# Kernel optimization log

Measured on AMD Instinct MI355X. Metric: run time of the kernel, lower is better.

Reference implementation:

```python
import jax, jax.numpy as jnp
import numpy as np

B, S, D = 32, 1024, 1024


def setup_inputs() -> dict:
    key = jax.random.key(0)
    ks = jax.random.split(key, 4)
    scale = 1.0 / np.sqrt(D)
    x = jax.random.normal(ks[0], (B, S, D), dtype=jnp.float32)
    Wg = jax.random.normal(ks[1], (D, D), dtype=jnp.float32) * scale
    Ws = jax.random.normal(ks[2], (D, D), dtype=jnp.float32) * scale
    Wi = jax.random.normal(ks[3], (D, D), dtype=jnp.float32) * scale
    bg = jnp.zeros((D,), jnp.float32)
    bs = jnp.zeros((D,), jnp.float32)
    bi = jnp.zeros((D,), jnp.float32)
    return {"x": x, "Wg": Wg, "bg": bg, "Ws": Ws, "bs": bs, "Wi": Wi, "bi": bi}


def reference(x, Wg, bg, Ws, bs, Wi, bi):
    # ContractiveSequenceMixer scan:
    #   gate_t = sigmoid(x_t @ Wg.T + bg)        (input-only: precomputable)
    #   mix_t  = h @ Ws.T + bs + (x_t @ Wi.T + bi)
    #   h      = gate_t * mix_t + (1 - gate_t) * h
    #   emit_t = h
    gates = jax.nn.sigmoid(jnp.einsum('bsd,ed->bse', x, Wg) + bg)  # [B,S,D]
    pin = jnp.einsum('bsd,ed->bse', x, Wi) + bi                     # [B,S,D]

    def step(state, gp):
        g, p = gp  # each [B, D]
        mix = state @ Ws.T + bs + p
        next_state = g * mix + (1.0 - g) * state
        return next_state, next_state

    init = jnp.zeros((x.shape[0], x.shape[2]), x.dtype)
    # time-major for scan
    final_state, outs = jax.lax.scan(
        step, init, (jnp.swapaxes(gates, 0, 1), jnp.swapaxes(pin, 0, 1)))
    emitted = jnp.swapaxes(outs, 0, 1)  # [B, S, D]
    return emitted, final_state
```

## Files before the change

kernel.cpp:

```cpp
#include <hip/hip_runtime.h>
#include <cstdint>


#define BATCH 32
#define SEQ   1024
#define DIM   1024
static const size_t BSD = (size_t)BATCH * SEQ * DIM;

typedef short  s16x8 __attribute__((ext_vector_type(8)));
typedef unsigned short u16x4 __attribute__((ext_vector_type(4)));
typedef float  f32x4 __attribute__((ext_vector_type(4)));

__device__ __forceinline__ unsigned short f2bf(float f) {
  union { float f; unsigned int u; } v; v.f = f;
  unsigned int r = v.u + 0x7fffu + ((v.u >> 16) & 1u);
  return (unsigned short)(r >> 16);
}
__device__ __forceinline__ float bf2f(unsigned short h) {
  union { unsigned int u; float f; } v; v.u = ((unsigned int)h) << 16; return v.f;
}

__device__ __forceinline__ void gload_lds16(const void* g, void* l) {
  __builtin_amdgcn_global_load_lds(
      (const __attribute__((address_space(1))) void*)g,
      (__attribute__((address_space(3))) void*)l, 16, 0, 0);
}

#define HLOAD(dst, base, IMM)                                              \
  asm volatile("global_load_dwordx4 %0, %1, off offset:" IMM " sc0 sc1"    \
               : "=v"(dst) : "v"(base))
#define HL8(arr, base)        \
  HLOAD(arr[0], base, "0");   \
  HLOAD(arr[1], base, "64");  \
  HLOAD(arr[2], base, "128"); \
  HLOAD(arr[3], base, "192"); \
  HLOAD(arr[4], base, "256"); \
  HLOAD(arr[5], base, "320"); \
  HLOAD(arr[6], base, "384"); \
  HLOAD(arr[7], base, "448")

__device__ __forceinline__ void cstore8(void* p, u16x4 v) {
  asm volatile("global_store_dwordx2 %0, %1, off sc0 sc1"
               :: "v"(p), "v"(v) : "memory");
}
__device__ __forceinline__ void cstore4(void* p, int v) {
  asm volatile("global_store_dword %0, %1, off sc0 sc1"
               :: "v"(p), "v"(v) : "memory");
}
__device__ __forceinline__ void cstore4u(void* p, unsigned v) {
  asm volatile("global_store_dword %0, %1, off sc0 sc1"
               :: "v"(p), "v"(v) : "memory");
}
__device__ __forceinline__ int cload4(const void* p) {
  int v;
  asm volatile("global_load_dword %0, %1, off sc0 sc1\n\ts_waitcnt vmcnt(0)"
               : "=v"(v) : "v"(p) : "memory");
  return v;
}

__global__ void split_x_kernel(const float* __restrict__ x,
                               unsigned short* __restrict__ xh,
                               unsigned short* __restrict__ xl, long n4) {
  long i = (long)blockIdx.x * blockDim.x + threadIdx.x;
  const long stride = (long)gridDim.x * blockDim.x;
  for (; i < n4; i += stride) {
    f32x4 v = *(const f32x4*)&x[i * 4];
    u16x4 vh, vl;
#pragma unroll
    for (int j = 0; j < 4; ++j) {
      unsigned short hb = f2bf(v[j]);
      vh[j] = hb; vl[j] = f2bf(v[j] - bf2f(hb));
    }
    *(u16x4*)&xh[i * 4] = vh;
    *(u16x4*)&xl[i * 4] = vl;
  }
}

__global__ void split_w_kernel(const float* __restrict__ Wg,
                               const float* __restrict__ Wi,
                               unsigned short* __restrict__ wh,
                               unsigned short* __restrict__ wl) {
  long i = (long)blockIdx.x * blockDim.x + threadIdx.x;
  if (i >= (long)(2048 * 1024 / 4)) return;
  long flat = i * 4;
  int row = (int)(flat >> 10);
  int col = (int)(flat & 1023);
  const float* src = (row < 1024) ? &Wg[(size_t)row * 1024 + col]
                                  : &Wi[(size_t)(row - 1024) * 1024 + col];
  f32x4 v = *(const f32x4*)src;
  u16x4 vh, vl;
#pragma unroll
  for (int j = 0; j < 4; ++j) {
    unsigned short hb = f2bf(v[j]);
    vh[j] = hb; vl[j] = f2bf(v[j] - bf2f(hb));
  }
  *(u16x4*)&wh[flat] = vh;
  *(u16x4*)&wl[flat] = vl;
}

__global__ void init_kernel(unsigned short* h_hi, unsigned short* h_lo,
                            int* flags) {
  int i = blockIdx.x * blockDim.x + threadIdx.x;
  u16x4 z4 = {0, 0, 0, 0};
  if (i < 16384) {
    cstore8(h_hi + (size_t)i * 4, z4);
    cstore8(h_lo + (size_t)i * 4, z4);
  }
  if (i < 4096) cstore4(flags + i, 0);
}

__global__ __launch_bounds__(256) void gemm_gp_kernel(
    const unsigned short* __restrict__ xh, const unsigned short* __restrict__ xl,
    const unsigned short* __restrict__ wh, const unsigned short* __restrict__ wl,
    const float* __restrict__ bg, const float* __restrict__ bi,
    float* __restrict__ G, float* __restrict__ P) {
  __shared__ unsigned short sAh[128 * 32], sAl[128 * 32], sBh[128 * 32], sBl[128 * 32];
  const int tid = threadIdx.x;
  const int w = tid >> 6, l = tid & 63;
  const int wr = w >> 1, wc = w & 1;
  const int lr = l & 15, lk8 = (l >> 4) * 8;
  const size_t rBase = (size_t)blockIdx.x * 128;
  const int cBase = blockIdx.y * 128;

  f32x4 acc[4][4];
  f32x4 z = {0.f, 0.f, 0.f, 0.f};
#pragma unroll
  for (int m = 0; m < 4; ++m)
#pragma unroll
    for (int n = 0; n < 4; ++n) acc[m][n] = z;

  for (int kb = 0; kb < 32; ++kb) {
    const int k0 = kb * 32;
#pragma unroll
    for (int i = 0; i < 2; ++i) {
      const int chunk = w * 128 + i * 64 + l;
      const int row = chunk >> 2;
      const int c8 = (chunk & 3) * 8;
      gload_lds16(xh + (rBase + row) * 1024 + k0 + c8, &sAh[chunk * 8]);
      gload_lds16(xl + (rBase + row) * 1024 + k0 + c8, &sAl[chunk * 8]);
      gload_lds16(wh + (size_t)(cBase + row) * 1024 + k0 + c8, &sBh[chunk * 8]);
      gload_lds16(wl + (size_t)(cBase + row) * 1024 + k0 + c8, &sBl[chunk * 8]);
    }
    __syncthreads();

    s16x8 ah[4], al[4], bh[4], bl[4];
#pragma unroll
    for (int m = 0; m < 4; ++m) {
      ah[m] = *(const s16x8*)&sAh[(wr * 64 + m * 16 + lr) * 32 + lk8];
      al[m] = *(const s16x8*)&sAl[(wr * 64 + m * 16 + lr) * 32 + lk8];
    }
#pragma unroll
    for (int n = 0; n < 4; ++n) {
      bh[n] = *(const s16x8*)&sBh[(wc * 64 + n * 16 + lr) * 32 + lk8];
      bl[n] = *(const s16x8*)&sBl[(wc * 64 + n * 16 + lr) * 32 + lk8];
    }
#pragma unroll
    for (int m = 0; m < 4; ++m)
#pragma unroll
      for (int n = 0; n < 4; ++n)
        acc[m][n] = __builtin_amdgcn_mfma_f32_16x16x32_bf16(ah[m], bh[n], acc[m][n], 0, 0, 0);
#pragma unroll
    for (int m = 0; m < 4; ++m)
#pragma unroll
      for (int n = 0; n < 4; ++n)
        acc[m][n] = __builtin_amdgcn_mfma_f32_16x16x32_bf16(al[m], bh[n], acc[m][n], 0, 0, 0);
#pragma unroll
    for (int m = 0; m < 4; ++m)
#pragma unroll
      for (int n = 0; n < 4; ++n)
        acc[m][n] = __builtin_amdgcn_mfma_f32_16x16x32_bf16(ah[m], bl[n], acc[m][n], 0, 0, 0);
    __syncthreads();
  }

  const bool isG = (cBase < 1024);
#pragma unroll
  for (int m = 0; m < 4; ++m) {
#pragma unroll
    for (int n = 0; n < 4; ++n) {
      const int col = cBase + wc * 64 + n * 16 + lr;
      const size_t row0 = rBase + wr * 64 + m * 16 + (l >> 4) * 4;
#pragma unroll
      for (int i = 0; i < 4; ++i) {
        float v = acc[m][n][i];
        if (isG) {
          v += bg[col];
          v = 1.f / (1.f + expf(-v));
          G[(row0 + i) * 1024 + col] = v;
        } else {
          v += bi[col - 1024];
          P[(row0 + i) * 1024 + (col - 1024)] = v;
        }
      }
    }
  }
}

__global__ __launch_bounds__(256) void recur_kernel(
    const float* __restrict__ Ws, const float* __restrict__ bs,
    const float* __restrict__ G, float* out,
    unsigned short* h_hi, unsigned short* h_lo, int* flags) {
  __shared__ float part[2 * 4 * 4 * 32];
  const int g = blockIdx.x >> 5;
  const int rank = blockIdx.x & 31;
  const int tid = threadIdx.x;
  const int kq = tid >> 6, l = tid & 63;
  const int lr = l & 15, lh4 = l >> 4;

  s16x8 bhi[2][8], blo[2][8];
#pragma unroll
  for (int nt = 0; nt < 2; ++nt) {
#pragma unroll
    for (int c = 0; c < 8; ++c) {
      const int e = rank * 32 + nt * 16 + lr;
      const int k = kq * 256 + c * 32 + lh4 * 8;
      const float* src = Ws + (size_t)e * DIM + k;
      f32x4 v0 = *(const f32x4*)src;
      f32x4 v1 = *(const f32x4*)(src + 4);
      s16x8 vh, vl;
#pragma unroll
      for (int j = 0; j < 4; ++j) {
        unsigned short hb = f2bf(v0[j]);
        vh[j] = (short)hb;
        vl[j] = (short)f2bf(v0[j] - bf2f(hb));
        unsigned short hb2 = f2bf(v1[j]);
        vh[4 + j] = (short)hb2;
        vl[4 + j] = (short)f2bf(v1[j] - bf2f(hb2));
      }
      bhi[nt][c] = vh; blo[nt][c] = vl;
    }
  }

  float hold0 = 0.f, hold1 = 0.f;
  float2 bs2 = {0.f, 0.f};
  size_t gpi = 0;
  int bgl = 0, egl = 0;
  if (tid < 64) {
    bgl = g * 4 + lh4;
    egl = rank * 32 + lr * 2;
    bs2 = *(const float2*)&bs[egl];
    gpi = ((size_t)bgl * SEQ) * DIM + egl;
  }
  float2 gA = {0, 0}, pA = {0, 0}, gB = {0, 0}, pB = {0, 0};
  if (tid < 64) { gA = *(const float2*)&G[gpi]; pA = *(const float2*)&out[gpi]; }

  const int lane_off = lr * 1024 + kq * 256 + lh4 * 8;
  const int* fp = flags + ((g << 5) + (kq << 3) + (l & 7)) * 16;
  int* myflag = flags + ((g << 5) + rank) * 16;

  auto body = [&](int t, float2& gc, float2& pc, float2& gn, float2& pn) {
    {
      int v;
      do { v = cload4(fp); } while (__any(v < t));
    }
    __builtin_amdgcn_sched_barrier(0);

    const unsigned short* Hh =
        h_hi + (size_t)(((t & 1) * 8 + g) * 4) * 1024 + lane_off;
    const unsigned short* Hl =
        h_lo + (size_t)(((t & 1) * 8 + g) * 4) * 1024 + lane_off;
    s16x8 ah[8], al[8];
    if (lr < 4) {
      HL8(ah, Hh);
      HL8(al, Hl);
    } else {
      s16x8 z8 = {0, 0, 0, 0, 0, 0, 0, 0};
#pragma unroll
      for (int c = 0; c < 8; ++c) { ah[c] = z8; al[c] = z8; }
    }
    asm volatile("s_waitcnt vmcnt(0)" ::: "memory");
    __builtin_amdgcn_sched_barrier(0);

    if (tid < 64) {
      const size_t gpn = gpi + ((t + 1 < SEQ) ? DIM : 0);
      gn = *(const float2*)&G[gpn];
      pn = *(const float2*)&out[gpn];
    }

    f32x4 z = {0.f, 0.f, 0.f, 0.f};
    f32x4 aA[2], aB[2], aC[2];
#pragma unroll
    for (int nt = 0; nt < 2; ++nt) { aA[nt] = z; aB[nt] = z; aC[nt] = z; }
#pragma unroll
    for (int c = 0; c < 8; ++c) {
#pragma unroll
      for (int nt = 0; nt < 2; ++nt) {
        aA[nt] = __builtin_amdgcn_mfma_f32_16x16x32_bf16(ah[c], bhi[nt][c], aA[nt], 0, 0, 0);
        aB[nt] = __builtin_amdgcn_mfma_f32_16x16x32_bf16(al[c], bhi[nt][c], aB[nt], 0, 0, 0);
        aC[nt] = __builtin_amdgcn_mfma_f32_16x16x32_bf16(ah[c], blo[nt][c], aC[nt], 0, 0, 0);
      }
    }

    if (lh4 == 0) {
#pragma unroll
      for (int nt = 0; nt < 2; ++nt) {
        f32x4 v = aA[nt] + aB[nt] + aC[nt];
#pragma unroll
        for (int i = 0; i < 4; ++i)
          part[(t & 1) * 512 + kq * 128 + i * 32 + nt * 16 + lr] = v[i];
      }
    }
    asm volatile("s_waitcnt lgkmcnt(0)" ::: "memory");
    __builtin_amdgcn_s_barrier();
    __builtin_amdgcn_sched_barrier(0);

    if (tid < 64) {
      const int b = lh4, e2 = lr * 2;
      const float* pp = &part[(t & 1) * 512 + b * 32 + e2];
      float2 r0 = *(const float2*)&pp[0];
      float2 r1 = *(const float2*)&pp[128];
      float2 r2 = *(const float2*)&pp[256];
      float2 r3 = *(const float2*)&pp[384];
      const float s0 = r0.x + r1.x + r2.x + r3.x;
      const float s1 = r0.y + r1.y + r2.y + r3.y;
      const float mix0 = s0 + bs2.x + pc.x;
      const float mix1 = s1 + bs2.y + pc.y;
      const float h0 = gc.x * mix0 + (1.f - gc.x) * hold0;
      const float h1 = gc.y * mix1 + (1.f - gc.y) * hold1;
      hold0 = h0; hold1 = h1;

      const unsigned short hb0 = f2bf(h0), hb1 = f2bf(h1);
      const unsigned short lb0 = f2bf(h0 - bf2f(hb0)), lb1 = f2bf(h1 - bf2f(hb1));
      const size_t hoff =
          (size_t)((((t + 1) & 1) * 8 + g) * 4 + b) * 1024 + egl;
      cstore4u(h_hi + hoff, (unsigned)hb0 | ((unsigned)hb1 << 16));
      cstore4u(h_lo + hoff, (unsigned)lb0 | ((unsigned)lb1 << 16));
      asm volatile("s_waitcnt vmcnt(0)" ::: "memory");
      if (l == 0 && t < SEQ - 1) cstore4(myflag, t + 1);

      float2 ev; ev.x = h0; ev.y = h1;
      *(float2*)&out[gpi] = ev;
      if (t == SEQ - 1)
        *(float2*)&out[BSD + (size_t)bgl * DIM + egl] = ev;
      gpi += ((t + 1 < SEQ) ? DIM : 0);
    }
  };

#pragma unroll 1
  for (int t = 0; t < SEQ; t += 2) {
    body(t, gA, pA, gB, pB);
    body(t + 1, gB, pB, gA, pA);
  }
}

extern "C" void kernel_launch(void* const* d_in, const int* in_sizes, int n_in,
                              void* d_out, int out_size, void* d_ws, size_t ws_size,
                              hipStream_t stream) {
  (void)in_sizes; (void)n_in; (void)out_size; (void)ws_size;
  const float* x  = (const float*)d_in[0];
  const float* Wg = (const float*)d_in[1];
  const float* bg = (const float*)d_in[2];
  const float* Ws = (const float*)d_in[3];
  const float* bs = (const float*)d_in[4];
  const float* Wi = (const float*)d_in[5];
  const float* bi = (const float*)d_in[6];
  float* out = (float*)d_out;
  char* ws = (char*)d_ws;

  unsigned short* xh   = (unsigned short*)(ws);
  unsigned short* xl   = (unsigned short*)(ws + 67108864);
  unsigned short* wh   = (unsigned short*)(ws + 134217728);
  unsigned short* wl   = (unsigned short*)(ws + 138412032);
  float*          G    = (float*)(ws + 142606336);
  unsigned short* h_hi = (unsigned short*)(ws + 276824064);
  unsigned short* h_lo = (unsigned short*)(ws + 276955136);
  int*            flags= (int*)(ws + 134217728);

  hipLaunchKernelGGL(split_x_kernel, dim3(4096), dim3(256), 0, stream,
                     x, xh, xl, (long)(BSD / 4));
  hipLaunchKernelGGL(split_w_kernel, dim3(2048), dim3(256), 0, stream, Wg, Wi, wh, wl);
  hipLaunchKernelGGL(gemm_gp_kernel, dim3(256, 16), dim3(256), 0, stream,
                     xh, xl, wh, wl, bg, bi, G, out);
  hipLaunchKernelGGL(init_kernel, dim3(64), dim3(256), 0, stream, h_hi, h_lo, flags);
  hipLaunchKernelGGL(recur_kernel, dim3(256), dim3(256), 0, stream,
                     Ws, bs, G, out, h_hi, h_lo, flags);
}
```

Before: 3.786 ms.

## Replace flag-based step sync with sentinel-tagged per-timestep hidden-state buffers

Drops the separate flag store and poll. Each step's packed hi/lo bf16 hidden state now goes to its own slot in a large history buffer that is pre-filled with a NaN sentinel, and consumers poll the data itself until no sentinel remains. This cuts one round trip per step: no waitcnt plus flag store on the producer side and no separate flag load before the data load. In exchange it adds a 128MB sentinel-fill pass that reuses the xh/xl workspace region, and it relies on a computed value never matching the sentinel bit pattern.

```diff
diff --git a/kernel.cpp b/kernel.cpp
--- a/kernel.cpp
+++ b/kernel.cpp
@@ -10,6 +10,10 @@
 typedef short  s16x8 __attribute__((ext_vector_type(8)));
 typedef unsigned short u16x4 __attribute__((ext_vector_type(4)));
 typedef float  f32x4 __attribute__((ext_vector_type(4)));
+typedef unsigned u32x4 __attribute__((ext_vector_type(4)));
+typedef unsigned u32x2 __attribute__((ext_vector_type(2)));
+
+#define SENT 0xFFC0FFC0u
 
 __device__ __forceinline__ unsigned short f2bf(float f) {
   union { float f; unsigned int u; } v; v.f = f;
@@ -26,36 +30,16 @@
       (__attribute__((address_space(3))) void*)l, 16, 0, 0);
 }
 
-#define HLOAD(dst, base, IMM)                                              \
+#define PLOAD(dst, base, IMM)                                              \
   asm volatile("global_load_dwordx4 %0, %1, off offset:" IMM " sc0 sc1"    \
                : "=v"(dst) : "v"(base))
-#define HL8(arr, base)        \
-  HLOAD(arr[0], base, "0");   \
-  HLOAD(arr[1], base, "64");  \
-  HLOAD(arr[2], base, "128"); \
-  HLOAD(arr[3], base, "192"); \
-  HLOAD(arr[4], base, "256"); \
-  HLOAD(arr[5], base, "320"); \
-  HLOAD(arr[6], base, "384"); \
-  HLOAD(arr[7], base, "448")
-
-__device__ __forceinline__ void cstore8(void* p, u16x4 v) {
+__device__ __forceinline__ void cstore8u(void* p, u32x2 v) {
   asm volatile("global_store_dwordx2 %0, %1, off sc0 sc1"
                :: "v"(p), "v"(v) : "memory");
 }
-__device__ __forceinline__ void cstore4(void* p, int v) {
-  asm volatile("global_store_dword %0, %1, off sc0 sc1"
+__device__ __forceinline__ void cstore16u(void* p, u32x4 v) {
+  asm volatile("global_store_dwordx4 %0, %1, off sc0 sc1"
                :: "v"(p), "v"(v) : "memory");
-}
-__device__ __forceinline__ void cstore4u(void* p, unsigned v) {
-  asm volatile("global_store_dword %0, %1, off sc0 sc1"
-               :: "v"(p), "v"(v) : "memory");
-}
-__device__ __forceinline__ int cload4(const void* p) {
-  int v;
-  asm volatile("global_load_dword %0, %1, off sc0 sc1\n\ts_waitcnt vmcnt(0)"
-               : "=v"(v) : "v"(p) : "memory");
-  return v;
 }
 
 __global__ void split_x_kernel(const float* __restrict__ x,
@@ -98,15 +82,15 @@
   *(u16x4*)&wl[flat] = vl;
 }
 
-__global__ void init_kernel(unsigned short* h_hi, unsigned short* h_lo,
-                            int* flags) {
-  int i = blockIdx.x * blockDim.x + threadIdx.x;
-  u16x4 z4 = {0, 0, 0, 0};
-  if (i < 16384) {
-    cstore8(h_hi + (size_t)i * 4, z4);
-    cstore8(h_lo + (size_t)i * 4, z4);
-  }
-  if (i < 4096) cstore4(flags + i, 0);
+__global__ void sentinel_kernel(unsigned* hs) {
+  long i = (long)blockIdx.x * blockDim.x + threadIdx.x;
+  const long stride = (long)gridDim.x * blockDim.x;
+  u32x4 z = {0u, 0u, 0u, 0u};
+  u32x4 s = {SENT, SENT, SENT, SENT};
+  for (; i < 8388608; i += stride) {
+    u32x4 v = (i < 8192) ? z : s;
+    cstore16u(hs + i * 4, v);
+  }
 }
 
 __global__ __launch_bounds__(256) void gemm_gp_kernel(
@@ -195,10 +179,9 @@
   }
 }
 
-__global__ __launch_bounds__(256) void recur_kernel(
+__global__ __launch_bounds__(256, 1) void recur_kernel(
     const float* __restrict__ Ws, const float* __restrict__ bs,
-    const float* __restrict__ G, float* out,
-    unsigned short* h_hi, unsigned short* h_lo, int* flags) {
+    const float* __restrict__ G, float* out, unsigned* hs) {
   __shared__ float part[2 * 4 * 4 * 32];
   const int g = blockIdx.x >> 5;
   const int rank = blockIdx.x & 31;
@@ -243,32 +226,56 @@
   float2 gA = {0, 0}, pA = {0, 0}, gB = {0, 0}, pB = {0, 0};
   if (tid < 64) { gA = *(const float2*)&G[gpi]; pA = *(const float2*)&out[gpi]; }
 
-  const int lane_off = lr * 1024 + kq * 256 + lh4 * 8;
-  const int* fp = flags + ((g << 5) + (kq << 3) + (l & 7)) * 16;
-  int* myflag = flags + ((g << 5) + rank) * 16;
+  const int cbase = (g * 4 + lr) * 1024 + kq * 256 + lh4 * 8;
+  const int sbase = bgl * 1024 + egl;
 
   auto body = [&](int t, float2& gc, float2& pc, float2& gn, float2& pn) {
-    {
-      int v;
-      do { v = cload4(fp); } while (__any(v < t));
-    }
+    const unsigned* hb = hs + (size_t)t * 32768 + cbase;
+    u32x4 pk[16];
+    int bad;
+    do {
+      if (lr < 4) {
+        PLOAD(pk[0], hb, "0");    PLOAD(pk[1], hb, "16");
+        PLOAD(pk[2], hb, "128");  PLOAD(pk[3], hb, "144");
+        PLOAD(pk[4], hb, "256");  PLOAD(pk[5], hb, "272");
+        PLOAD(pk[6], hb, "384");  PLOAD(pk[7], hb, "400");
+        PLOAD(pk[8], hb, "512");  PLOAD(pk[9], hb, "528");
+        PLOAD(pk[10], hb, "640"); PLOAD(pk[11], hb, "656");
+        PLOAD(pk[12], hb, "768"); PLOAD(pk[13], hb, "784");
+        PLOAD(pk[14], hb, "896"); PLOAD(pk[15], hb, "912");
+      }
+      asm volatile("s_waitcnt vmcnt(0)" ::: "memory");
+      bad = 0;
+      if (lr < 4) {
+#pragma unroll
+        for (int i = 0; i < 16; ++i)
+#pragma unroll
+          for (int j = 0; j < 4; ++j) bad |= (pk[i][j] == SENT);
+      }
+    } while (__any(bad));
     __builtin_amdgcn_sched_barrier(0);
 
-    const unsigned short* Hh =
-        h_hi + (size_t)(((t & 1) * 8 + g) * 4) * 1024 + lane_off;
-    const unsigned short* Hl =
-        h_lo + (size_t)(((t & 1) * 8 + g) * 4) * 1024 + lane_off;
     s16x8 ah[8], al[8];
     if (lr < 4) {
-      HL8(ah, Hh);
-      HL8(al, Hl);
+#pragma unroll
+      for (int c = 0; c < 8; ++c) {
+        u32x4 a = pk[2 * c], b2 = pk[2 * c + 1];
+        union { unsigned u[4]; s16x8 v; } hh, ll;
+        hh.u[0] = (a[0] >> 16) | (a[1] & 0xFFFF0000u);
+        hh.u[1] = (a[2] >> 16) | (a[3] & 0xFFFF0000u);
+        hh.u[2] = (b2[0] >> 16) | (b2[1] & 0xFFFF0000u);
+        hh.u[3] = (b2[2] >> 16) | (b2[3] & 0xFFFF0000u);
+        ll.u[0] = (a[0] & 0xFFFFu) | (a[1] << 16);
+        ll.u[1] = (a[2] & 0xFFFFu) | (a[3] << 16);
+        ll.u[2] = (b2[0] & 0xFFFFu) | (b2[1] << 16);
+        ll.u[3] = (b2[2] & 0xFFFFu) | (b2[3] << 16);
+        ah[c] = hh.v; al[c] = ll.v;
+      }
     } else {
       s16x8 z8 = {0, 0, 0, 0, 0, 0, 0, 0};
 #pragma unroll
       for (int c = 0; c < 8; ++c) { ah[c] = z8; al[c] = z8; }
     }
-    asm volatile("s_waitcnt vmcnt(0)" ::: "memory");
-    __builtin_amdgcn_sched_barrier(0);
 
     if (tid < 64) {
       const size_t gpn = gpi + ((t + 1 < SEQ) ? DIM : 0);
@@ -318,14 +325,15 @@
       const float h1 = gc.y * mix1 + (1.f - gc.y) * hold1;
       hold0 = h0; hold1 = h1;
 
-      const unsigned short hb0 = f2bf(h0), hb1 = f2bf(h1);
-      const unsigned short lb0 = f2bf(h0 - bf2f(hb0)), lb1 = f2bf(h1 - bf2f(hb1));
-      const size_t hoff =
-          (size_t)((((t + 1) & 1) * 8 + g) * 4 + b) * 1024 + egl;
-      cstore4u(h_hi + hoff, (unsigned)hb0 | ((unsigned)hb1 << 16));
-      cstore4u(h_lo + hoff, (unsigned)lb0 | ((unsigned)lb1 << 16));
-      asm volatile("s_waitcnt vmcnt(0)" ::: "memory");
-      if (l == 0 && t < SEQ - 1) cstore4(myflag, t + 1);
+      if (t < SEQ - 1) {
+        const unsigned short hb0 = f2bf(h0), hb1 = f2bf(h1);
+        const unsigned short lb0 = f2bf(h0 - bf2f(hb0));
+        const unsigned short lb1 = f2bf(h1 - bf2f(hb1));
+        u32x2 pv;
+        pv[0] = ((unsigned)hb0 << 16) | (unsigned)lb0;
+        pv[1] = ((unsigned)hb1 << 16) | (unsigned)lb1;
+        cstore8u(hs + (size_t)(t + 1) * 32768 + sbase, pv);
+      }
 
       float2 ev; ev.x = h0; ev.y = h1;
       *(float2*)&out[gpi] = ev;
@@ -356,21 +364,19 @@
   float* out = (float*)d_out;
   char* ws = (char*)d_ws;
 
-  unsigned short* xh   = (unsigned short*)(ws);
-  unsigned short* xl   = (unsigned short*)(ws + 67108864);
-  unsigned short* wh   = (unsigned short*)(ws + 134217728);
-  unsigned short* wl   = (unsigned short*)(ws + 138412032);
-  float*          G    = (float*)(ws + 142606336);
-  unsigned short* h_hi = (unsigned short*)(ws + 276824064);
-  unsigned short* h_lo = (unsigned short*)(ws + 276955136);
-  int*            flags= (int*)(ws + 134217728);
+  unsigned short* xh = (unsigned short*)(ws);
+  unsigned short* xl = (unsigned short*)(ws + 67108864);
+  unsigned short* wh = (unsigned short*)(ws + 134217728);
+  unsigned short* wl = (unsigned short*)(ws + 138412032);
+  float*          G  = (float*)(ws + 142606336);
+  unsigned*       hs = (unsigned*)(ws);
 
   hipLaunchKernelGGL(split_x_kernel, dim3(4096), dim3(256), 0, stream,
                      x, xh, xl, (long)(BSD / 4));
   hipLaunchKernelGGL(split_w_kernel, dim3(2048), dim3(256), 0, stream, Wg, Wi, wh, wl);
   hipLaunchKernelGGL(gemm_gp_kernel, dim3(256, 16), dim3(256), 0, stream,
                      xh, xl, wh, wl, bg, bi, G, out);
-  hipLaunchKernelGGL(init_kernel, dim3(64), dim3(256), 0, stream, h_hi, h_lo, flags);
+  hipLaunchKernelGGL(sentinel_kernel, dim3(4096), dim3(256), 0, stream, hs);
   hipLaunchKernelGGL(recur_kernel, dim3(256), dim3(256), 0, stream,
-                     Ws, bs, G, out, h_hi, h_lo, flags);
-}
+                     Ws, bs, G, out, hs);
+}
```

New measurement: 4.703 ms. 1.24x slower.

## Use sentinel-filled per-step hidden-state history to drop store drain before flag

Applied to the files above, without the earlier changes.

The two-slot hidden-state ping-pong buffer becomes a full per-timestep history, stored over the no-longer-needed split-x workspace and prefilled with a NaN sentinel pattern. Writers no longer wait for their hidden-state stores to complete before raising the progress flag. Readers still poll the flags, then check the loaded data for the sentinel and reload until real values arrive. This removes a store-completion wait from every step of the serial recurrence. In exchange it adds a large sentinel-fill pass over two 64 MB buffers and a validation loop per step.

```diff
diff --git a/kernel.cpp b/kernel.cpp
--- a/kernel.cpp
+++ b/kernel.cpp
@@ -10,6 +10,9 @@
 typedef short  s16x8 __attribute__((ext_vector_type(8)));
 typedef unsigned short u16x4 __attribute__((ext_vector_type(4)));
 typedef float  f32x4 __attribute__((ext_vector_type(4)));
+typedef unsigned u32x4 __attribute__((ext_vector_type(4)));
+
+#define SENT 0xFFC0FFC0u
 
 __device__ __forceinline__ unsigned short f2bf(float f) {
   union { float f; unsigned int u; } v; v.f = f;
@@ -39,16 +42,16 @@
   HLOAD(arr[6], base, "384"); \
   HLOAD(arr[7], base, "448")
 
-__device__ __forceinline__ void cstore8(void* p, u16x4 v) {
-  asm volatile("global_store_dwordx2 %0, %1, off sc0 sc1"
+__device__ __forceinline__ void cstore4u(void* p, unsigned v) {
+  asm volatile("global_store_dword %0, %1, off sc0 sc1"
                :: "v"(p), "v"(v) : "memory");
 }
 __device__ __forceinline__ void cstore4(void* p, int v) {
   asm volatile("global_store_dword %0, %1, off sc0 sc1"
                :: "v"(p), "v"(v) : "memory");
 }
-__device__ __forceinline__ void cstore4u(void* p, unsigned v) {
-  asm volatile("global_store_dword %0, %1, off sc0 sc1"
+__device__ __forceinline__ void cstore16u(void* p, u32x4 v) {
+  asm volatile("global_store_dwordx4 %0, %1, off sc0 sc1"
                :: "v"(p), "v"(v) : "memory");
 }
 __device__ __forceinline__ int cload4(const void* p) {
@@ -56,6 +59,11 @@
   asm volatile("global_load_dword %0, %1, off sc0 sc1\n\ts_waitcnt vmcnt(0)"
                : "=v"(v) : "v"(p) : "memory");
   return v;
+}
+
+__device__ __forceinline__ int is_sent(s16x8 v) {
+  union { s16x8 s; u32x4 u; } x; x.s = v;
+  return (x.u[0] == SENT) | (x.u[1] == SENT) | (x.u[2] == SENT) | (x.u[3] == SENT);
 }
 
 __global__ void split_x_kernel(const float* __restrict__ x,
@@ -98,13 +106,15 @@
   *(u16x4*)&wl[flat] = vl;
 }
 
-__global__ void init_kernel(unsigned short* h_hi, unsigned short* h_lo,
-                            int* flags) {
-  int i = blockIdx.x * blockDim.x + threadIdx.x;
-  u16x4 z4 = {0, 0, 0, 0};
-  if (i < 16384) {
-    cstore8(h_hi + (size_t)i * 4, z4);
-    cstore8(h_lo + (size_t)i * 4, z4);
+__global__ void sentinel_kernel(unsigned* hsH, unsigned* hsL, int* flags) {
+  long i = (long)blockIdx.x * blockDim.x + threadIdx.x;
+  const long stride = (long)gridDim.x * blockDim.x;
+  u32x4 z = {0u, 0u, 0u, 0u};
+  u32x4 s = {SENT, SENT, SENT, SENT};
+  for (long k = i; k < 4194304; k += stride) {
+    u32x4 v = (k < 4096) ? z : s;
+    cstore16u(hsH + k * 4, v);
+    cstore16u(hsL + k * 4, v);
   }
   if (i < 4096) cstore4(flags + i, 0);
 }
@@ -198,7 +208,7 @@
 __global__ __launch_bounds__(256) void recur_kernel(
     const float* __restrict__ Ws, const float* __restrict__ bs,
     const float* __restrict__ G, float* out,
-    unsigned short* h_hi, unsigned short* h_lo, int* flags) {
+    unsigned short* hsH, unsigned short* hsL, int* flags) {
   __shared__ float part[2 * 4 * 4 * 32];
   const int g = blockIdx.x >> 5;
   const int rank = blockIdx.x & 31;
@@ -243,7 +253,8 @@
   float2 gA = {0, 0}, pA = {0, 0}, gB = {0, 0}, pB = {0, 0};
   if (tid < 64) { gA = *(const float2*)&G[gpi]; pA = *(const float2*)&out[gpi]; }
 
-  const int lane_off = lr * 1024 + kq * 256 + lh4 * 8;
+  const int cbase = (g * 4 + lr) * 1024 + kq * 256 + lh4 * 8;
+  const int sbase = bgl * 1024 + egl;
   const int* fp = flags + ((g << 5) + (kq << 3) + (l & 7)) * 16;
   int* myflag = flags + ((g << 5) + rank) * 16;
 
@@ -254,10 +265,8 @@
     }
     __builtin_amdgcn_sched_barrier(0);
 
-    const unsigned short* Hh =
-        h_hi + (size_t)(((t & 1) * 8 + g) * 4) * 1024 + lane_off;
-    const unsigned short* Hl =
-        h_lo + (size_t)(((t & 1) * 8 + g) * 4) * 1024 + lane_off;
+    const unsigned short* Hh = hsH + (size_t)t * 32768 + cbase;
+    const unsigned short* Hl = hsL + (size_t)t * 32768 + cbase;
     s16x8 ah[8], al[8];
     if (lr < 4) {
       HL8(ah, Hh);
@@ -267,7 +276,17 @@
 #pragma unroll
       for (int c = 0; c < 8; ++c) { ah[c] = z8; al[c] = z8; }
     }
-    asm volatile("s_waitcnt vmcnt(0)" ::: "memory");
+    for (;;) {
+      asm volatile("s_waitcnt vmcnt(0)" ::: "memory");
+      __builtin_amdgcn_sched_barrier(0);
+      int bad = 0;
+      if (lr < 4) {
+#pragma unroll
+        for (int c = 0; c < 8; ++c) bad |= is_sent(ah[c]) | is_sent(al[c]);
+      }
+      if (!__any(bad)) break;
+      if (lr < 4) { HL8(ah, Hh); HL8(al, Hl); }
+    }
     __builtin_amdgcn_sched_barrier(0);
 
     if (tid < 64) {
@@ -318,14 +337,15 @@
       const float h1 = gc.y * mix1 + (1.f - gc.y) * hold1;
       hold0 = h0; hold1 = h1;
 
-      const unsigned short hb0 = f2bf(h0), hb1 = f2bf(h1);
-      const unsigned short lb0 = f2bf(h0 - bf2f(hb0)), lb1 = f2bf(h1 - bf2f(hb1));
-      const size_t hoff =
-          (size_t)((((t + 1) & 1) * 8 + g) * 4 + b) * 1024 + egl;
-      cstore4u(h_hi + hoff, (unsigned)hb0 | ((unsigned)hb1 << 16));
-      cstore4u(h_lo + hoff, (unsigned)lb0 | ((unsigned)lb1 << 16));
-      asm volatile("s_waitcnt vmcnt(0)" ::: "memory");
-      if (l == 0 && t < SEQ - 1) cstore4(myflag, t + 1);
+      if (t < SEQ - 1) {
+        const unsigned short hb0 = f2bf(h0), hb1 = f2bf(h1);
+        const unsigned short lb0 = f2bf(h0 - bf2f(hb0));
+        const unsigned short lb1 = f2bf(h1 - bf2f(hb1));
+        const size_t so = (size_t)(t + 1) * 32768 + sbase;
+        cstore4u(hsH + so, (unsigned)hb0 | ((unsigned)hb1 << 16));
+        cstore4u(hsL + so, (unsigned)lb0 | ((unsigned)lb1 << 16));
+        if (l == 0) cstore4(myflag, t + 1);
+      }
 
       float2 ev; ev.x = h0; ev.y = h1;
       *(float2*)&out[gpi] = ev;
@@ -356,13 +376,13 @@
   float* out = (float*)d_out;
   char* ws = (char*)d_ws;
 
-  unsigned short* xh   = (unsigned short*)(ws);
-  unsigned short* xl   = (unsigned short*)(ws + 67108864);
-  unsigned short* wh   = (unsigned short*)(ws + 134217728);
-  unsigned short* wl   = (unsigned short*)(ws + 138412032);
-  float*          G    = (float*)(ws + 142606336);
-  unsigned short* h_hi = (unsigned short*)(ws + 276824064);
-  unsigned short* h_lo = (unsigned short*)(ws + 276955136);
+  unsigned short* xh = (unsigned short*)(ws);
+  unsigned short* xl = (unsigned short*)(ws + 67108864);
+  unsigned short* wh = (unsigned short*)(ws + 134217728);
+  unsigned short* wl = (unsigned short*)(ws + 138412032);
+  float*          G  = (float*)(ws + 142606336);
+  unsigned short* hsH  = (unsigned short*)(ws);
+  unsigned short* hsL  = (unsigned short*)(ws + 67108864);
   int*            flags= (int*)(ws + 134217728);
 
   hipLaunchKernelGGL(split_x_kernel, dim3(4096), dim3(256), 0, stream,
@@ -370,7 +390,8 @@
   hipLaunchKernelGGL(split_w_kernel, dim3(2048), dim3(256), 0, stream, Wg, Wi, wh, wl);
   hipLaunchKernelGGL(gemm_gp_kernel, dim3(256, 16), dim3(256), 0, stream,
                      xh, xl, wh, wl, bg, bi, G, out);
-  hipLaunchKernelGGL(init_kernel, dim3(64), dim3(256), 0, stream, h_hi, h_lo, flags);
+  hipLaunchKernelGGL(sentinel_kernel, dim3(4096), dim3(256), 0, stream,
+                     (unsigned*)hsH, (unsigned*)hsL, flags);
   hipLaunchKernelGGL(recur_kernel, dim3(256), dim3(256), 0, stream,
-                     Ws, bs, G, out, h_hi, h_lo, flags);
-}
+                     Ws, bs, G, out, hsH, hsL, flags);
+}
```

After: 3.883 ms. 2.6% more time.
